# Performance work log

Measured on AMD Instinct MI355X. Metric: run time of the kernel, lower is better.

## Reference

```python
import jax, jax.numpy as jnp
import numpy as np
from jax import lax

NUM_CLASSES = 5
NUM_TASKS = 20
CONV_CHANS = [(64, 3), (64, 64), (128, 64), (128, 128), (256, 128), (256, 256)]  # (out, in)


def setup_inputs() -> dict:
    key = jax.random.key(0)
    ks = jax.random.split(key, 16)
    B = 512
    x = jax.random.normal(ks[0], (B, 3, 32, 32), dtype=jnp.float32)
    tid = jax.random.randint(ks[1], (B,), 0, NUM_TASKS)
    inp = {"x": x, "tid": tid}
    for i, (oc, ic) in enumerate(CONV_CHANS):
        fan_in = ic * 9
        inp[f"w{i}"] = jax.random.normal(ks[2 + 2 * i], (oc, ic, 3, 3), dtype=jnp.float32) * np.float32((2.0 / fan_in) ** 0.5)
        inp[f"b{i}"] = jnp.zeros((oc,), dtype=jnp.float32)
    inp["cw"] = jax.random.normal(ks[14], (NUM_CLASSES * NUM_TASKS, 4096), dtype=jnp.float32) * np.float32(4096 ** -0.5)
    inp["cb"] = jnp.zeros((NUM_CLASSES * NUM_TASKS,), dtype=jnp.float32)
    return inp


def _conv_relu(x, w, b):
    y = lax.conv_general_dilated(x, w, window_strides=(1, 1), padding='SAME',
                                 dimension_numbers=('NCHW', 'OIHW', 'NCHW'))
    return jax.nn.relu(y + b[None, :, None, None])


def _maxpool2(x):
    return lax.reduce_window(x, -jnp.inf, lax.max, (1, 1, 2, 2), (1, 1, 2, 2), 'VALID')


def _forward(x, tid, ws, bs, cw, cb):
    # VGG cfg [64,64,'M',128,128,'M',256,256,'M']
    h = _conv_relu(x, ws[0], bs[0])
    h = _conv_relu(h, ws[1], bs[1])
    h = _maxpool2(h)
    h = _conv_relu(h, ws[2], bs[2])
    h = _conv_relu(h, ws[3], bs[3])
    h = _maxpool2(h)
    h = _conv_relu(h, ws[4], bs[4])
    h = _conv_relu(h, ws[5], bs[5])
    h = _maxpool2(h)                      # [B, 256, 4, 4]
    feat = h.reshape(h.shape[0], -1)      # [B, 4096], matches torch NCHW flatten
    # Batched task-indexed classifier: gather each sample's 5-row weight block.
    w_sel = cw.reshape(NUM_TASKS, NUM_CLASSES, 4096)[tid]   # [B, 5, 4096]
    b_sel = cb.reshape(NUM_TASKS, NUM_CLASSES)[tid]         # [B, 5]
    return jnp.einsum('bcd,bd->bc', w_sel, feat) + b_sel


def reference(x, tid, w0, b0, w1, b1, w2, b2, w3, b3, w4, b4, w5, b5, cw, cb):
    ws = (w0, w1, w2, w3, w4, w5)
    bs = (b0, b1, b2, b3, b4, b5)
    return _forward(x, tid, ws, bs, cw, cb)
```

## Files before the change

### kernel.cpp

```cpp
#include <hip/hip_runtime.h>


typedef __attribute__((ext_vector_type(8))) short short8;
typedef __attribute__((ext_vector_type(4))) float floatx4;
typedef unsigned int uint;
typedef unsigned short ushort;

__device__ __forceinline__ ushort f2bf(float f) {
    uint u = __float_as_uint(f);
    return (ushort)((u + 0x7fffu + ((u >> 16) & 1u)) >> 16);
}
__device__ __forceinline__ float bf2f(ushort h) {
    return __uint_as_float(((uint)h) << 16);
}

typedef const __attribute__((address_space(1))) unsigned int* gas_ptr;
typedef __attribute__((address_space(3))) unsigned int* las_ptr;
__device__ __forceinline__ void gload_lds16(const void* g, void* l) {
    __builtin_amdgcn_global_load_lds((gas_ptr)g, (las_ptr)l, 16, 0, 0);
}

__device__ __forceinline__ void wlin_one(
    const float* __restrict__ src, short* __restrict__ dst, int OC, int IC, int o)
{
    int j    = o & 7;
    int lane = (o >> 3) & 63;
    int r    = o >> 9;
    int G16  = OC >> 4;
    int g    = r % G16;  r /= G16;
    int kk   = r % 9;
    int icb  = r / 9;
    int oc = g * 16 + (lane & 15);
    int ic = icb * 32 + (lane >> 4) * 8 + j;
    dst[o] = (short)f2bf(src[((long)oc * IC + ic) * 9 + kk]);
}

#define N_W0 2048
#define N_W1 36864
#define N_W2 73728
#define N_W3 147456
#define N_W4 294912
#define N_W5 589824
#define N_WT_TOTAL (N_W0 + N_W1 + N_W2 + N_W3 + N_W4 + N_W5)

__global__ __launch_bounds__(256) void wtransform_all(
    const float* __restrict__ w0, const float* __restrict__ w1,
    const float* __restrict__ w2, const float* __restrict__ w3,
    const float* __restrict__ w4, const float* __restrict__ w5,
    short* __restrict__ wt0, short* __restrict__ wts1, short* __restrict__ wts2,
    short* __restrict__ wts3, short* __restrict__ wts4, short* __restrict__ wts5,
    short* __restrict__ zp)
{
    if (blockIdx.x == 0 && threadIdx.x < 32) zp[threadIdx.x] = 0;
    int idx = blockIdx.x * 256 + threadIdx.x;
    if (idx < N_W0) {
        int oc = idx >> 5, k = idx & 31;
        wt0[idx] = (k < 27) ? (short)f2bf(w0[oc * 27 + k]) : (short)0;
        return;
    }
    idx -= N_W0;
    if (idx < N_W1) { wlin_one(w1, wts1, 64, 64, idx); return; }
    idx -= N_W1;
    if (idx < N_W2) { wlin_one(w2, wts2, 128, 64, idx); return; }
    idx -= N_W2;
    if (idx < N_W3) { wlin_one(w3, wts3, 128, 128, idx); return; }
    idx -= N_W3;
    if (idx < N_W4) { wlin_one(w4, wts4, 256, 128, idx); return; }
    idx -= N_W4;
    wlin_one(w5, wts5, 256, 256, idx);
}

__global__ __launch_bounds__(256, 2) void conv0_mfma(
    const float* __restrict__ x, const short* __restrict__ wT0,
    const float* __restrict__ b0, ushort* __restrict__ out)
{
    __shared__ float  s_x[3 * 18 * 34];
    __shared__ ushort s_b[4 * 512 * 8];

    const int tid  = threadIdx.x;
    const int wv   = tid >> 6;
    const int lane = tid & 63;
    const int quad = lane >> 4;
    const int l16  = lane & 15;
    const int b    = blockIdx.x >> 1;
    const int r0   = (blockIdx.x & 1) * 16;

    for (int idx = tid; idx < 3 * 18 * 34; idx += 256) {
        int c   = idx / 612;
        int rem = idx - c * 612;
        int ry  = rem / 34, rx = rem - ry * 34;
        int gy  = r0 + ry - 1, gx = rx - 1;
        float v = 0.f;
        if (gy >= 0 && gy < 32 && gx >= 0 && gx < 32)
            v = x[(((long)b * 3 + c) * 32 + gy) * 32 + gx];
        s_x[idx] = v;
    }
    __syncthreads();

#pragma unroll
    for (int rep = 0; rep < 2; ++rep) {
        int pxl = rep * 256 + tid;
        int py = pxl >> 5, px = pxl & 31;
        ushort v[32];
#pragma unroll
        for (int c = 0; c < 3; ++c)
#pragma unroll
            for (int ky = 0; ky < 3; ++ky)
#pragma unroll
                for (int kx = 0; kx < 3; ++kx)
                    v[c * 9 + ky * 3 + kx] = f2bf(s_x[c * 612 + (py + ky) * 34 + (px + kx)]);
#pragma unroll
        for (int k = 27; k < 32; ++k) v[k] = 0;
#pragma unroll
        for (int q = 0; q < 4; ++q)
            *(uint4*)(&s_b[(q * 512 + pxl) * 8]) = *(const uint4*)(v + q * 8);
    }
    __syncthreads();

    floatx4 acc[4][8];
#pragma unroll
    for (int i = 0; i < 4; ++i)
#pragma unroll
        for (int t = 0; t < 8; ++t) acc[i][t] = (floatx4)0.f;

    short8 afr[4];
#pragma unroll
    for (int i = 0; i < 4; ++i)
        afr[i] = *(const short8*)(wT0 + (i * 16 + l16) * 32 + quad * 8);
#pragma unroll
    for (int t = 0; t < 8; ++t) {
        int pxl = wv * 128 + t * 16 + l16;
        short8 bfr = *(const short8*)(&s_b[(quad * 512 + pxl) * 8]);
#pragma unroll
        for (int i = 0; i < 4; ++i)
            acc[i][t] = __builtin_amdgcn_mfma_f32_16x16x32_bf16(afr[i], bfr, acc[i][t], 0, 0, 0);
    }

#pragma unroll
    for (int i = 0; i < 4; ++i) {
        int oc0 = i * 16 + quad * 4;
        float4 bv = *(const float4*)(b0 + oc0);
#pragma unroll
        for (int t = 0; t < 8; ++t) {
            int pxl = wv * 128 + t * 16 + l16;
            int py = pxl >> 5, px = pxl & 31;
            long dst = ((((long)b * 8 + (oc0 >> 3)) * 32 + r0 + py) * 32 + px) * 8 + (oc0 & 7);
            float v0 = acc[i][t][0] + bv.x;
            float v1 = acc[i][t][1] + bv.y;
            float v2 = acc[i][t][2] + bv.z;
            float v3 = acc[i][t][3] + bv.w;
            ushort o[4];
            o[0] = f2bf(v0 > 0.f ? v0 : 0.f);
            o[1] = f2bf(v1 > 0.f ? v1 : 0.f);
            o[2] = f2bf(v2 > 0.f ? v2 : 0.f);
            o[3] = f2bf(v3 > 0.f ? v3 : 0.f);
            *(uint2*)(out + dst) = *(uint2*)o;
        }
    }
}

template<int IC, int OC, int H, int W, int ROWS, int OCGROUPS, bool POOL>
__global__ __launch_bounds__(256, 3) void conv_so(
    const ushort* __restrict__ act_in,
    const short*  __restrict__ wTs,
    const float*  __restrict__ bias,
    ushort* __restrict__ act_out,
    const ushort* __restrict__ zp)
{
    constexpr int WPAD  = W + 2;
    constexpr int RPAD  = ROWS + 2;
    constexpr int UNITS = RPAD * WPAD;
    constexpr int SEGS  = H / ROWS;
    constexpr int C8I   = IC / 8;
    constexpr int G16   = OC / 16;
    constexpr int NICB  = IC / 32;
    constexpr int C8O   = OC / 8;
    constexpr int TMAX  = NICB * 9;
    constexpr int NSTG  = UNITS * C8I;

    __shared__ ushort s_act[NSTG * 8];

    const int tid  = threadIdx.x;
    const int wv   = tid >> 6;
    const int lane = tid & 63;
    const int quad = lane >> 4;
    const int l16  = lane & 15;

    const int b   = blockIdx.x / SEGS;
    const int seg = blockIdx.x - b * SEGS;
    const int r0  = seg * ROWS;
    const int ocg = wv % OCGROUPS;
    const int pxg = wv / OCGROUPS;

    for (int c = tid; c < NSTG; c += 256) {
        int sub  = c / UNITS;
        int unit = c - sub * UNITS;
        int ry   = unit / WPAD, cx = unit - ry * WPAD;
        int gy   = r0 + ry - 1, gx = cx - 1;
        const ushort* src = zp;
        if ((unsigned)gy < (unsigned)H && (unsigned)gx < (unsigned)W)
            src = act_in + ((((long)b * C8I + sub) * H + gy) * W + gx) * 8;
        gload_lds16(src, &s_act[(size_t)(c - lane) * 8]);
    }
    __syncthreads();

    floatx4 acc[4][4];
#pragma unroll
    for (int i = 0; i < 4; ++i)
#pragma unroll
        for (int t = 0; t < 4; ++t) acc[i][t] = (floatx4)0.f;

    int bbase[4];
#pragma unroll
    for (int t = 0; t < 4; ++t) {
        int pxl = pxg * 64 + t * 16 + l16;
        int py  = pxl / W, px = pxl - py * W;
        bbase[t] = (py * WPAD + px) * 8;
    }

    const short8* wb = (const short8*)wTs;
    const int  wbase = (ocg * 4) * 64 + lane;
    const long WSTEP = (long)G16 * 64;

    short8 wpipe[3][4];
#pragma unroll
    for (int d = 0; d < 3; ++d)
#pragma unroll
        for (int i = 0; i < 4; ++i)
            wpipe[d][i] = wb[(long)d * WSTEP + wbase + i * 64];

    int tl = 0;
    for (int icb = 0; icb < NICB; ++icb) {
#pragma unroll
        for (int kk = 0; kk < 9; ++kk) {
            const int ky = kk / 3, kx = kk - ky * 3;
            const int koff = ((icb * 4 + quad) * UNITS + ky * WPAD + kx) * 8;
            short8 bfr[4];
#pragma unroll
            for (int t = 0; t < 4; ++t)
                bfr[t] = *(const short8*)(&s_act[bbase[t] + koff]);
            const int slot = kk % 3;
#pragma unroll
            for (int i = 0; i < 4; ++i)
#pragma unroll
                for (int t = 0; t < 4; ++t)
                    acc[i][t] = __builtin_amdgcn_mfma_f32_16x16x32_bf16(
                        wpipe[slot][i], bfr[t], acc[i][t], 0, 0, 0);
            int tn = tl + 3;
            if (tn >= TMAX) tn = 0;
#pragma unroll
            for (int i = 0; i < 4; ++i)
                wpipe[slot][i] = wb[(long)tn * WSTEP + wbase + i * 64];
            ++tl;
        }
    }

    if constexpr (!POOL) {
#pragma unroll
        for (int i = 0; i < 4; ++i) {
            int oc0 = ocg * 64 + i * 16 + quad * 4;
            float4 bv = *(const float4*)(bias + oc0);
#pragma unroll
            for (int t = 0; t < 4; ++t) {
                int pxl = pxg * 64 + t * 16 + l16;
                int py  = pxl / W, px = pxl - py * W;
                long dst = ((((long)b * C8O + (oc0 >> 3)) * H + r0 + py) * W + px) * 8 + (oc0 & 7);
                float v0 = acc[i][t][0] + bv.x;
                float v1 = acc[i][t][1] + bv.y;
                float v2 = acc[i][t][2] + bv.z;
                float v3 = acc[i][t][3] + bv.w;
                ushort o[4];
                o[0] = f2bf(v0 > 0.f ? v0 : 0.f);
                o[1] = f2bf(v1 > 0.f ? v1 : 0.f);
                o[2] = f2bf(v2 > 0.f ? v2 : 0.f);
                o[3] = f2bf(v3 > 0.f ? v3 : 0.f);
                *(uint2*)(act_out + dst) = *(uint2*)o;
            }
        }
    } else {
        __syncthreads();
        ushort* s_pool = s_act;
        constexpr int PSTR = OC + 8;
        static_assert(ROWS * W * PSTR <= NSTG * 8, "pool scratch fits");
#pragma unroll
        for (int i = 0; i < 4; ++i) {
            int oc0 = ocg * 64 + i * 16 + quad * 4;
            float4 bv = *(const float4*)(bias + oc0);
#pragma unroll
            for (int t = 0; t < 4; ++t) {
                int pxl = pxg * 64 + t * 16 + l16;
                float v0 = acc[i][t][0] + bv.x;
                float v1 = acc[i][t][1] + bv.y;
                float v2 = acc[i][t][2] + bv.z;
                float v3 = acc[i][t][3] + bv.w;
                ushort o[4];
                o[0] = f2bf(v0 > 0.f ? v0 : 0.f);
                o[1] = f2bf(v1 > 0.f ? v1 : 0.f);
                o[2] = f2bf(v2 > 0.f ? v2 : 0.f);
                o[3] = f2bf(v3 > 0.f ? v3 : 0.f);
                *(uint2*)(&s_pool[pxl * PSTR + oc0]) = *(uint2*)o;
            }
        }
        __syncthreads();
        constexpr int PH = ROWS / 2, PW = W / 2, HOT = H / 2;
        const int pr0 = r0 / 2;
        for (int u = tid; u < PH * PW * C8O; u += 256) {
            int c8 = u % C8O;
            int pp = u / C8O;
            int xo = pp % PW, yo = pp / PW;
            const ushort* p00 = &s_pool[((2 * yo) * W + 2 * xo) * PSTR + c8 * 8];
            uint4 q0 = *(const uint4*)(p00);
            uint4 q1 = *(const uint4*)(p00 + PSTR);
            uint4 q2 = *(const uint4*)(p00 + W * PSTR);
            uint4 q3 = *(const uint4*)(p00 + W * PSTR + PSTR);
            const ushort* a0 = (const ushort*)&q0;
            const ushort* a1 = (const ushort*)&q1;
            const ushort* a2 = (const ushort*)&q2;
            const ushort* a3 = (const ushort*)&q3;
            ushort r[8];
#pragma unroll
            for (int j = 0; j < 8; ++j) {
                ushort m0 = a0[j] > a1[j] ? a0[j] : a1[j];
                ushort m1 = a2[j] > a3[j] ? a2[j] : a3[j];
                r[j] = m0 > m1 ? m0 : m1;
            }
            long dst = ((((long)b * C8O + c8) * HOT + pr0 + yo) * PW + xo) * 8;
            *(uint4*)(act_out + dst) = *(uint4*)r;
        }
    }
}

__global__ __launch_bounds__(256) void classifier_k(
    const ushort* __restrict__ feat, const int* __restrict__ tids,
    const float* __restrict__ cw, const float* __restrict__ cb,
    float* __restrict__ out, int B)
{
    int g = blockIdx.x * 256 + threadIdx.x;
    int wid = g >> 6, lane = g & 63;
    if (wid >= B * 5) return;
    int b = wid / 5, c = wid - b * 5;
    int t = tids[b];
    const float* wrow = cw + (long)(t * 5 + c) * 4096;
    const ushort* f = feat + (long)b * 4096;
    float s = 0.f;
#pragma unroll 4
    for (int d = lane; d < 4096; d += 64) {
        int fidx = (((d >> 7) * 16) + (d & 15)) * 8 + ((d >> 4) & 7);
        s += wrow[d] * bf2f(f[fidx]);
    }
#pragma unroll
    for (int off = 32; off > 0; off >>= 1) s += __shfl_down(s, off, 64);
    if (lane == 0) out[wid] = s + cb[t * 5 + c];
}

extern "C" void kernel_launch(void* const* d_in, const int* in_sizes, int n_in,
                              void* d_out, int out_size, void* d_ws, size_t ws_size,
                              hipStream_t stream)
{
    const float* x   = (const float*)d_in[0];
    const int*   tid = (const int*)d_in[1];
    const float* w0 = (const float*)d_in[2];  const float* b0 = (const float*)d_in[3];
    const float* w1 = (const float*)d_in[4];  const float* b1 = (const float*)d_in[5];
    const float* w2 = (const float*)d_in[6];  const float* b2 = (const float*)d_in[7];
    const float* w3 = (const float*)d_in[8];  const float* b3 = (const float*)d_in[9];
    const float* w4 = (const float*)d_in[10]; const float* b4 = (const float*)d_in[11];
    const float* w5 = (const float*)d_in[12]; const float* b5 = (const float*)d_in[13];
    const float* cw = (const float*)d_in[14];
    const float* cb = (const float*)d_in[15];
    float* outp = (float*)d_out;

    const int B = in_sizes[0] / (3 * 32 * 32);

    short* wt0  = (short*)d_ws;
    short* wts1 = wt0 + N_W0;
    short* wts2 = wts1 + N_W1;
    short* wts3 = wts2 + N_W2;
    short* wts4 = wts3 + N_W3;
    short* wts5 = wts4 + N_W4;
    short* zp   = wts5 + N_W5;
    const size_t WT_HW = (size_t)N_WT_TOTAL + 32;
    const size_t fixed_bytes = WT_HW * 2;

    int Bc = B;
    while (Bc > 2 && fixed_bytes + (size_t)Bc * 2 * 65536 * 2 > ws_size) Bc >>= 1;
    if (Bc < 2) Bc = 2;

    ushort* bufA = (ushort*)((short*)d_ws + WT_HW);
    ushort* bufB = bufA + (size_t)Bc * 65536;

    wtransform_all<<<(N_WT_TOTAL + 255) / 256, 256, 0, stream>>>(
        w0, w1, w2, w3, w4, w5, wt0, wts1, wts2, wts3, wts4, wts5, zp);

    for (int cb0 = 0; cb0 < B; cb0 += Bc) {
        const float* xc = x + (size_t)cb0 * 3 * 32 * 32;
        const int* tidc = tid + cb0;
        float* outc = outp + (size_t)cb0 * 5;

        conv0_mfma<<<Bc * 2, 256, 0, stream>>>(xc, wt0, b0, bufA);
        conv_so<64, 64, 32, 32, 8, 1, true><<<Bc * 4, 256, 0, stream>>>(bufA, wts1, b1, bufB, (ushort*)zp);
        conv_so<64, 128, 16, 16, 8, 2, false><<<Bc * 2, 256, 0, stream>>>(bufB, wts2, b2, bufA, (ushort*)zp);
        conv_so<128, 128, 16, 16, 8, 2, true><<<Bc * 2, 256, 0, stream>>>(bufA, wts3, b3, bufB, (ushort*)zp);
        conv_so<128, 256, 8, 8, 8, 4, false><<<Bc, 256, 0, stream>>>(bufB, wts4, b4, bufA, (ushort*)zp);
        conv_so<256, 256, 8, 8, 8, 4, true><<<Bc, 256, 0, stream>>>(bufA, wts5, b5, bufB, (ushort*)zp);
        classifier_k<<<(Bc * 5 * 64 + 255) / 256, 256, 0, stream>>>(bufB, tidc, cw, cb, outc, Bc);
    }
}
```

Measured before the change: 268.0 us.

## Process two images per block in 8x8 conv layers to share weight loads

Adds a conv_so2 kernel for the two 8x8 layers (conv4, conv5) that uses 512-thread blocks, each handling two images. Waves 0-3 and 4-7 take the same output-channel groups on different images, so weight fragments fetched through a 3-deep register pipeline are shared across twice the pixels per block. The cost is more LDS per block (two staged images), fewer blocks in the grid, and a launch-bounds hint that may limit registers. It also relies on Bc being even.

```diff
diff --git a/kernel.cpp b/kernel.cpp
--- a/kernel.cpp
+++ b/kernel.cpp
@@ -330,6 +330,179 @@
     }
 }
 
+template<int IC, int OC, bool POOL>
+__global__ __launch_bounds__(512, 2) void conv_so2(
+    const ushort* __restrict__ act_in,
+    const short*  __restrict__ wTs,
+    const float*  __restrict__ bias,
+    ushort* __restrict__ act_out,
+    const ushort* __restrict__ zp)
+{
+    constexpr int H = 8, W = 8;
+    constexpr int WPAD  = 10;
+    constexpr int UNITS = 10 * 10;
+    constexpr int C8I   = IC / 8;
+    constexpr int G16   = OC / 16;
+    constexpr int NICB  = IC / 32;
+    constexpr int C8O   = OC / 8;
+    constexpr int TMAX  = NICB * 9;
+    constexpr int NSTG  = UNITS * C8I;
+
+    __shared__ ushort s_act[2 * NSTG * 8];
+
+    const int tid  = threadIdx.x;
+    const int wv   = tid >> 6;
+    const int lane = tid & 63;
+    const int quad = lane >> 4;
+    const int l16  = lane & 15;
+
+    const int ocg  = wv & 3;
+    const int img2 = wv >> 2;
+    const long b0i = (long)blockIdx.x * 2;
+
+    for (int c = tid; c < 2 * NSTG; c += 512) {
+        int img  = c / NSTG;
+        int cc   = c - img * NSTG;
+        int sub  = cc / UNITS;
+        int unit = cc - sub * UNITS;
+        int ry   = unit / WPAD, cx = unit - ry * WPAD;
+        int gy   = ry - 1, gx = cx - 1;
+        const ushort* src = zp;
+        if ((unsigned)gy < (unsigned)H && (unsigned)gx < (unsigned)W)
+            src = act_in + ((((b0i + img) * C8I + sub) * H + gy) * W + gx) * 8;
+        gload_lds16(src, &s_act[(size_t)(c - lane) * 8]);
+    }
+    __syncthreads();
+
+    floatx4 acc[4][4];
+#pragma unroll
+    for (int i = 0; i < 4; ++i)
+#pragma unroll
+        for (int t = 0; t < 4; ++t) acc[i][t] = (floatx4)0.f;
+
+    int bbase[4];
+#pragma unroll
+    for (int t = 0; t < 4; ++t) {
+        int pxl = t * 16 + l16;
+        int py  = pxl >> 3, px = pxl & 7;
+        bbase[t] = (py * WPAD + px) * 8 + img2 * NSTG * 8;
+    }
+
+    const short8* wb = (const short8*)wTs;
+    const int  wbase = (ocg * 4) * 64 + lane;
+    const long WSTEP = (long)G16 * 64;
+
+    short8 wpipe[3][4];
+#pragma unroll
+    for (int d = 0; d < 3; ++d)
+#pragma unroll
+        for (int i = 0; i < 4; ++i)
+            wpipe[d][i] = wb[(long)d * WSTEP + wbase + i * 64];
+
+    int tl = 0;
+    for (int icb = 0; icb < NICB; ++icb) {
+#pragma unroll
+        for (int kk = 0; kk < 9; ++kk) {
+            const int ky = kk / 3, kx = kk - ky * 3;
+            const int koff = ((icb * 4 + quad) * UNITS + ky * WPAD + kx) * 8;
+            short8 bfr[4];
+#pragma unroll
+            for (int t = 0; t < 4; ++t)
+                bfr[t] = *(const short8*)(&s_act[bbase[t] + koff]);
+            const int slot = kk % 3;
+#pragma unroll
+            for (int i = 0; i < 4; ++i)
+#pragma unroll
+                for (int t = 0; t < 4; ++t)
+                    acc[i][t] = __builtin_amdgcn_mfma_f32_16x16x32_bf16(
+                        wpipe[slot][i], bfr[t], acc[i][t], 0, 0, 0);
+            int tn = tl + 3;
+            if (tn >= TMAX) tn = 0;
+#pragma unroll
+            for (int i = 0; i < 4; ++i)
+                wpipe[slot][i] = wb[(long)tn * WSTEP + wbase + i * 64];
+            ++tl;
+        }
+    }
+
+    const long b = b0i + img2;
+    if constexpr (!POOL) {
+#pragma unroll
+        for (int i = 0; i < 4; ++i) {
+            int oc0 = ocg * 64 + i * 16 + quad * 4;
+            float4 bv = *(const float4*)(bias + oc0);
+#pragma unroll
+            for (int t = 0; t < 4; ++t) {
+                int pxl = t * 16 + l16;
+                int py  = pxl >> 3, px = pxl & 7;
+                long dst = (((b * C8O + (oc0 >> 3)) * H + py) * W + px) * 8 + (oc0 & 7);
+                float v0 = acc[i][t][0] + bv.x;
+                float v1 = acc[i][t][1] + bv.y;
+                float v2 = acc[i][t][2] + bv.z;
+                float v3 = acc[i][t][3] + bv.w;
+                ushort o[4];
+                o[0] = f2bf(v0 > 0.f ? v0 : 0.f);
+                o[1] = f2bf(v1 > 0.f ? v1 : 0.f);
+                o[2] = f2bf(v2 > 0.f ? v2 : 0.f);
+                o[3] = f2bf(v3 > 0.f ? v3 : 0.f);
+                *(uint2*)(act_out + dst) = *(uint2*)o;
+            }
+        }
+    } else {
+        __syncthreads();
+        ushort* s_pool = s_act;
+        constexpr int PSTR = OC + 8;
+        static_assert(H * W * PSTR <= NSTG * 8, "pool scratch fits per image");
+        ushort* my_pool = s_pool + (size_t)img2 * NSTG * 8;
+#pragma unroll
+        for (int i = 0; i < 4; ++i) {
+            int oc0 = ocg * 64 + i * 16 + quad * 4;
+            float4 bv = *(const float4*)(bias + oc0);
+#pragma unroll
+            for (int t = 0; t < 4; ++t) {
+                int pxl = t * 16 + l16;
+                float v0 = acc[i][t][0] + bv.x;
+                float v1 = acc[i][t][1] + bv.y;
+                float v2 = acc[i][t][2] + bv.z;
+                float v3 = acc[i][t][3] + bv.w;
+                ushort o[4];
+                o[0] = f2bf(v0 > 0.f ? v0 : 0.f);
+                o[1] = f2bf(v1 > 0.f ? v1 : 0.f);
+                o[2] = f2bf(v2 > 0.f ? v2 : 0.f);
+                o[3] = f2bf(v3 > 0.f ? v3 : 0.f);
+                *(uint2*)(&my_pool[pxl * PSTR + oc0]) = *(uint2*)o;
+            }
+        }
+        __syncthreads();
+        constexpr int PH = 4, PW = 4, HOT = 4;
+        for (int u = tid; u < 2 * PH * PW * C8O; u += 512) {
+            int img = u / (PH * PW * C8O);
+            int uu  = u - img * (PH * PW * C8O);
+            int c8 = uu % C8O;
+            int pp = uu / C8O;
+            int xo = pp % PW, yo = pp / PW;
+            const ushort* p00 = &s_pool[(size_t)img * NSTG * 8 + ((2 * yo) * W + 2 * xo) * PSTR + c8 * 8];
+            uint4 q0 = *(const uint4*)(p00);
+            uint4 q1 = *(const uint4*)(p00 + PSTR);
+            uint4 q2 = *(const uint4*)(p00 + W * PSTR);
+            uint4 q3 = *(const uint4*)(p00 + W * PSTR + PSTR);
+            const ushort* a0 = (const ushort*)&q0;
+            const ushort* a1 = (const ushort*)&q1;
+            const ushort* a2 = (const ushort*)&q2;
+            const ushort* a3 = (const ushort*)&q3;
+            ushort r[8];
+#pragma unroll
+            for (int j = 0; j < 8; ++j) {
+                ushort m0 = a0[j] > a1[j] ? a0[j] : a1[j];
+                ushort m1 = a2[j] > a3[j] ? a2[j] : a3[j];
+                r[j] = m0 > m1 ? m0 : m1;
+            }
+            long dst = ((((b0i + img) * C8O + c8) * HOT + yo) * PW + xo) * 8;
+            *(uint4*)(act_out + dst) = *(uint4*)r;
+        }
+    }
+}
+
 __global__ __launch_bounds__(256) void classifier_k(
     const ushort* __restrict__ feat, const int* __restrict__ tids,
     const float* __restrict__ cw, const float* __restrict__ cb,
@@ -400,8 +573,8 @@
         conv_so<64, 64, 32, 32, 8, 1, true><<<Bc * 4, 256, 0, stream>>>(bufA, wts1, b1, bufB, (ushort*)zp);
         conv_so<64, 128, 16, 16, 8, 2, false><<<Bc * 2, 256, 0, stream>>>(bufB, wts2, b2, bufA, (ushort*)zp);
         conv_so<128, 128, 16, 16, 8, 2, true><<<Bc * 2, 256, 0, stream>>>(bufA, wts3, b3, bufB, (ushort*)zp);
-        conv_so<128, 256, 8, 8, 8, 4, false><<<Bc, 256, 0, stream>>>(bufB, wts4, b4, bufA, (ushort*)zp);
-        conv_so<256, 256, 8, 8, 8, 4, true><<<Bc, 256, 0, stream>>>(bufA, wts5, b5, bufB, (ushort*)zp);
+        conv_so2<128, 256, false><<<Bc / 2, 512, 0, stream>>>(bufB, wts4, b4, bufA, (ushort*)zp);
+        conv_so2<256, 256, true><<<Bc / 2, 512, 0, stream>>>(bufA, wts5, b5, bufB, (ushort*)zp);
         classifier_k<<<(Bc * 5 * 64 + 255) / 256, 256, 0, stream>>>(bufB, tidc, cw, cb, outc, Bc);
     }
 }
```

Measured after the change: 315.5 us. +17.7%, slower.
